# Kernel optimization log

Measured on AMD Instinct MI355X. Metric: run time of the kernel, lower is better.

## Reference

```python
import jax, jax.numpy as jnp
import numpy as np

E = 2048      # embed_dim
HQ = 32       # num_query_heads
HKV = 8       # num_kv_heads
DH = E // HQ  # head_dim = 64
G = HQ // HKV # group_size = 4
KV_DIM = E * HKV // HQ  # 512
B, S = 2, 2048


def setup_inputs() -> dict:
    key = jax.random.key(0)
    ks = jax.random.split(key, 11)
    sc_in = 1.0 / np.sqrt(E)
    sc_attn = 1.0 / np.sqrt(E)
    return {
        "query": jax.random.normal(ks[0], (B, S, E), jnp.float32),
        "key": jax.random.normal(ks[1], (B, S, E), jnp.float32),
        "value": jax.random.normal(ks[2], (B, S, E), jnp.float32),
        "Wq": jax.random.normal(ks[3], (E, E), jnp.float32) * sc_in,
        "bq": jnp.zeros((E,), jnp.float32),
        "Wk": jax.random.normal(ks[4], (E, KV_DIM), jnp.float32) * sc_in,
        "bk": jnp.zeros((KV_DIM,), jnp.float32),
        "Wv": jax.random.normal(ks[5], (E, KV_DIM), jnp.float32) * sc_in,
        "bv": jnp.zeros((KV_DIM,), jnp.float32),
        "Wo": jax.random.normal(ks[6], (E, E), jnp.float32) * sc_attn,
        "bo": jnp.zeros((E,), jnp.float32),
    }


def reference(query, key, value, Wq, bq, Wk, bk, Wv, bv, Wo, bo):
    b, s, _ = query.shape
    # projections
    Q = (query @ Wq + bq).reshape(b, s, HQ, DH).transpose(0, 2, 1, 3)   # [B,HQ,S,DH]
    K = (key @ Wk + bk).reshape(b, s, HKV, DH).transpose(0, 2, 1, 3)    # [B,HKV,S,DH]
    V = (value @ Wv + bv).reshape(b, s, HKV, DH).transpose(0, 2, 1, 3)  # [B,HKV,S,DH]
    # GQA: repeat_interleave along head dim (kv head h -> query heads h*G..h*G+G-1)
    K = jnp.repeat(K, G, axis=1)  # [B,HQ,S,DH]
    V = jnp.repeat(V, G, axis=1)  # [B,HQ,S,DH]
    scores = jnp.einsum('bhqd,bhkd->bhqk', Q, K) / np.sqrt(DH).astype(np.float32)
    attn_weights = jax.nn.softmax(scores, axis=-1)                      # [B,HQ,S,S]
    attn_out = jnp.einsum('bhqk,bhkd->bhqd', attn_weights, V)           # [B,HQ,S,DH]
    attn_out = attn_out.transpose(0, 2, 1, 3).reshape(b, s, E)
    out = attn_out @ Wo + bo
    return out, attn_weights
```

## Files before the change

### kernel.cpp

```cpp
#include <hip/hip_runtime.h>
#include <stdint.h>

typedef _Float16 f16;
typedef _Float16 f16x8 __attribute__((ext_vector_type(8)));
typedef _Float16 f16x4 __attribute__((ext_vector_type(4)));
typedef float    f32x4 __attribute__((ext_vector_type(4)));

#define SEQ   2048
#define EDIM  2048
#define NHQ   32
#define NHKV  8
#define DHEAD 64
#define KVD   512
#define NB    2
#define NTOK  (NB*SEQ)
#define SCALE 0.1803368801111204f

__device__ __forceinline__ f32x4 mfma16(f16x8 a, f16x8 b, f32x4 c) {
  return __builtin_amdgcn_mfma_f32_16x16x32_f16(a, b, c, 0, 0, 0);
}

__device__ __forceinline__ void gload_lds16(const void* g, void* l) {
  __builtin_amdgcn_global_load_lds(
      (const __attribute__((address_space(1))) void*)g,
      (__attribute__((address_space(3))) void*)l, 16, 0, 0);
}

__global__ __launch_bounds__(256) void k_cvt3(const float* __restrict__ s0,
                                              const float* __restrict__ s1,
                                              const float* __restrict__ s2,
                                              f16* __restrict__ d) {
  int i = blockIdx.x * 256 + threadIdx.x;
  int t = i >> 21, j = i & ((1 << 21) - 1);
  const float* s = (t == 0) ? s0 : ((t == 1) ? s1 : s2);
  float4 v = reinterpret_cast<const float4*>(s)[j];
  f16x4 h;
  h[0] = (f16)v.x; h[1] = (f16)v.y; h[2] = (f16)v.z; h[3] = (f16)v.w;
  reinterpret_cast<f16x4*>(d)[i] = h;
}

__global__ __launch_bounds__(256) void k_tconv(const float* __restrict__ s0,
                                               const float* __restrict__ s1,
                                               f16* __restrict__ d0,
                                               f16* __restrict__ d1,
                                               int R, int C) {
  const float* s = blockIdx.z ? s1 : s0;
  f16* d = blockIdx.z ? d1 : d0;
  __shared__ float t[32][33];
  int tr = blockIdx.x, tc = blockIdx.y;
  int lr = threadIdx.x >> 3;
  int lc = (threadIdx.x & 7) << 2;
  float4 v = *reinterpret_cast<const float4*>(&s[(size_t)(tr*32+lr)*C + tc*32 + lc]);
  t[lr][lc+0] = v.x; t[lr][lc+1] = v.y; t[lr][lc+2] = v.z; t[lr][lc+3] = v.w;
  __syncthreads();
  f16x4 h;
  h[0] = (f16)t[lc+0][lr];
  h[1] = (f16)t[lc+1][lr];
  h[2] = (f16)t[lc+2][lr];
  h[3] = (f16)t[lc+3][lr];
  *reinterpret_cast<f16x4*>(&d[(size_t)(tc*32+lr)*R + tr*32 + lc]) = h;
}

__global__ __launch_bounds__(256) void k_trv(const f16* __restrict__ src,
                                             f16* __restrict__ dst) {
  __shared__ f16 t[64][68];
  int bh = blockIdx.x;
  int st = blockIdx.y;
  int b = bh >> 3, h = bh & 7;
  #pragma unroll
  for (int i = 0; i < 4; ++i) {
    int sl = i*16 + (threadIdx.x >> 4);
    int d4 = (threadIdx.x & 15) * 4;
    *(f16x4*)&t[sl][d4] =
        *(const f16x4*)&src[(size_t)(b*SEQ + st*64 + sl)*KVD + h*DHEAD + d4];
  }
  __syncthreads();
  #pragma unroll
  for (int i = 0; i < 4; ++i) {
    int dl = i*16 + (threadIdx.x >> 4);
    int s4 = (threadIdx.x & 15) * 4;
    f16x4 v;
    v[0] = t[s4+0][dl]; v[1] = t[s4+1][dl]; v[2] = t[s4+2][dl]; v[3] = t[s4+3][dl];
    *(f16x4*)&dst[(size_t)(bh*DHEAD + dl)*SEQ + st*64 + s4] = v;
  }
}

template<int F16OUT>
__global__ __launch_bounds__(256) void k_gemm(
    const f16* __restrict__ A0, const f16* __restrict__ A1,
    const f16* __restrict__ Bt0, const f16* __restrict__ Bt1,
    const float* __restrict__ bias0, const float* __restrict__ bias1,
    void* __restrict__ C0, void* __restrict__ C1,
    int M, int N, int K)
{
  const f16* A    = blockIdx.z ? A1 : A0;
  const f16* Bt   = blockIdx.z ? Bt1 : Bt0;
  const float* bias = blockIdx.z ? bias1 : bias0;
  void* Cout      = blockIdx.z ? C1 : C0;

  __shared__ f16 sA[128*64];
  __shared__ f16 sB[128*64];
  const int tid  = threadIdx.x;
  const int lane = tid & 63, wv = tid >> 6;
  const int tn = blockIdx.x, tm = blockIdx.y;
  const int wm = wv >> 1, wn = wv & 1;
  const int l15 = lane & 15, lhi = lane >> 4;

  const f32x4 zz = {0.f, 0.f, 0.f, 0.f};
  f32x4 acc[4][4];
  #pragma unroll
  for (int m = 0; m < 4; ++m)
    #pragma unroll
    for (int n = 0; n < 4; ++n) acc[m][n] = zz;

  const f16* gsrc[8];
  f16* ldst[8];
  #pragma unroll
  for (int i = 0; i < 8; ++i) {
    int u = wv*8 + i;
    int r  = (u & 15)*8 + (lane >> 3);
    int cb = ((lane & 7) << 4) ^ ((r & 7) << 4);
    if (u < 16) {
      gsrc[i] = A  + (size_t)(tm*128 + r)*K + (cb >> 1);
      ldst[i] = sA + u*512;
    } else {
      gsrc[i] = Bt + (size_t)(tn*128 + r)*K + (cb >> 1);
      ldst[i] = sB + (u - 16)*512;
    }
  }

  int aoff[2][4], boff[2][4];
  #pragma unroll
  for (int ks = 0; ks < 2; ++ks)
    #pragma unroll
    for (int m = 0; m < 4; ++m) {
      int ra = wm*64 + m*16 + l15;
      aoff[ks][m] = ra*128 + ((ks*64 + (lhi << 4)) ^ ((ra & 7) << 4));
      int rb = wn*64 + m*16 + l15;
      boff[ks][m] = rb*128 + ((ks*64 + (lhi << 4)) ^ ((rb & 7) << 4));
    }

  const int nkb = K >> 6;
  for (int kb = 0; kb < nkb; ++kb) {
    #pragma unroll
    for (int i = 0; i < 8; ++i)
      gload_lds16(gsrc[i] + kb*64, ldst[i]);
    __syncthreads();
    #pragma unroll
    for (int ks = 0; ks < 2; ++ks) {
      f16x8 af[4], bf[4];
      #pragma unroll
      for (int m = 0; m < 4; ++m)
        af[m] = *(const f16x8*)((const char*)sA + aoff[ks][m]);
      #pragma unroll
      for (int n = 0; n < 4; ++n)
        bf[n] = *(const f16x8*)((const char*)sB + boff[ks][n]);
      #pragma unroll
      for (int m = 0; m < 4; ++m)
        #pragma unroll
        for (int n = 0; n < 4; ++n)
          acc[m][n] = mfma16(af[m], bf[n], acc[m][n]);
    }
    __syncthreads();
  }

  float bcol[4];
  #pragma unroll
  for (int n = 0; n < 4; ++n)
    bcol[n] = bias[tn*128 + wn*64 + n*16 + l15];
  #pragma unroll
  for (int m = 0; m < 4; ++m)
    #pragma unroll
    for (int n = 0; n < 4; ++n)
      #pragma unroll
      for (int r = 0; r < 4; ++r) {
        int row = tm*128 + wm*64 + m*16 + lhi*4 + r;
        int col = tn*128 + wn*64 + n*16 + l15;
        float v = acc[m][n][r] + bcol[n];
        if (F16OUT) ((f16*)Cout)[(size_t)row*N + col] = (f16)v;
        else        ((float*)Cout)[(size_t)row*N + col] = v;
      }
}

__global__ __launch_bounds__(256) void k_attn(
    const f16* __restrict__ Qp,
    const f16* __restrict__ Kp,
    const f16* __restrict__ Vt,
    float* __restrict__ wout,
    f16* __restrict__ AO)
{
  __shared__ f16 sK[2][64*64];
  __shared__ f16 sV[2][64*64];
  __shared__ f16 sW[4][16*64];
  const int tid = threadIdx.x, lane = tid & 63, wv = tid >> 6;
  const int bid = (blockIdx.x & 7) * 256 + (blockIdx.x >> 3);
  const int b = bid >> 10, h = (bid >> 5) & 31, qb = bid & 31;
  const int hk = h >> 2;
  const int l15 = lane & 15, lhi = lane >> 4;
  const int rloc = (lane >> 3) & 7, chk = lane & 7;
  const int csw = (chk ^ rloc) * 8;
  const int sw  = (l15 & 7) << 4;
  const int qrow0 = qb*64 + wv*16;
  const f32x4 zz = {0.f, 0.f, 0.f, 0.f};

  f16x8 qf[2];
  #pragma unroll
  for (int ks = 0; ks < 2; ++ks)
    qf[ks] = *(const f16x8*)&Qp[(size_t)(b*SEQ + qrow0 + l15)*EDIM
                                + h*DHEAD + ks*32 + lhi*8];

  const f16* Kb = Kp + (size_t)(b*SEQ)*KVD + hk*DHEAD;
  const f16* Vb = Vt + (size_t)((b*NHKV + hk)*DHEAD)*SEQ;

  float lsum = 0.f;
  {
    #pragma unroll
    for (int i = 0; i < 2; ++i) {
      int u = wv*2 + i;
      gload_lds16(Kb + (size_t)(u*8 + rloc)*KVD + csw, &sK[0][u*512]);
    }
    __syncthreads();
    int buf = 0;
    for (int kb = 0; kb < SEQ/64; ++kb) {
      if (kb < SEQ/64 - 1) {
        #pragma unroll
        for (int i = 0; i < 2; ++i) {
          int u = wv*2 + i;
          gload_lds16(Kb + (size_t)((kb+1)*64 + u*8 + rloc)*KVD + csw, &sK[buf^1][u*512]);
        }
      }
      #pragma unroll
      for (int kt = 0; kt < 4; ++kt) {
        const char* kbase = (const char*)&sK[buf][0] + (kt*16 + l15)*128;
        f16x8 kf0 = *(const f16x8*)(kbase + ((lhi*16) ^ sw));
        f16x8 kf1 = *(const f16x8*)(kbase + ((64 + lhi*16) ^ sw));
        f32x4 s = zz;
        s = mfma16(kf0, qf[0], s);
        s = mfma16(kf1, qf[1], s);
        #pragma unroll
        for (int r = 0; r < 4; ++r)
          lsum += __builtin_amdgcn_exp2f(s[r] * SCALE);
      }
      __syncthreads();
      buf ^= 1;
    }
  }
  float den = lsum;
  den += __shfl_xor(den, 16);
  den += __shfl_xor(den, 32);
  const float rinv = __builtin_amdgcn_rcpf(den);

  f32x4 o[4];
  #pragma unroll
  for (int dt = 0; dt < 4; ++dt) o[dt] = zz;

  f16* swv = &sW[wv][0];
  float* wrow = wout + (size_t)((b*NHQ + h)*SEQ + qrow0)*SEQ;

  {
    #pragma unroll
    for (int i = 0; i < 2; ++i) {
      int u = wv*2 + i;
      gload_lds16(Kb + (size_t)(u*8 + rloc)*KVD + csw, &sK[0][u*512]);
      gload_lds16(Vb + (size_t)(u*8 + rloc)*SEQ + csw, &sV[0][u*512]);
    }
    __syncthreads();
    int buf = 0;
    for (int kb = 0; kb < SEQ/64; ++kb) {
      if (kb < SEQ/64 - 1) {
        #pragma unroll
        for (int i = 0; i < 2; ++i) {
          int u = wv*2 + i;
          gload_lds16(Kb + (size_t)((kb+1)*64 + u*8 + rloc)*KVD + csw, &sK[buf^1][u*512]);
          gload_lds16(Vb + (size_t)(u*8 + rloc)*SEQ + (kb+1)*64 + csw, &sV[buf^1][u*512]);
        }
      }
      #pragma unroll
      for (int kt = 0; kt < 4; ++kt) {
        const char* kbase = (const char*)&sK[buf][0] + (kt*16 + l15)*128;
        f16x8 kf0 = *(const f16x8*)(kbase + ((lhi*16) ^ sw));
        f16x8 kf1 = *(const f16x8*)(kbase + ((64 + lhi*16) ^ sw));
        f32x4 s = zz;
        s = mfma16(kf0, qf[0], s);
        s = mfma16(kf1, qf[1], s);
        f32x4 wvec;
        f16x4 wh;
        #pragma unroll
        for (int r = 0; r < 4; ++r) {
          float w = __builtin_amdgcn_exp2f(s[r] * SCALE) * rinv;
          wvec[r] = w;
          wh[r] = (f16)w;
        }
        __builtin_nontemporal_store(wvec,
            (f32x4*)(wrow + (size_t)l15*SEQ + kb*64 + kt*16 + lhi*4));
        *(f16x4*)((char*)swv + l15*128 + ((kt*32 + lhi*8) ^ sw)) = wh;
      }
      #pragma unroll
      for (int ks = 0; ks < 2; ++ks) {
        f16x8 af = *(const f16x8*)((const char*)swv + l15*128 + ((ks*64 + lhi*16) ^ sw));
        #pragma unroll
        for (int dt = 0; dt < 4; ++dt) {
          const char* vbase = (const char*)&sV[buf][0] + (dt*16 + l15)*128;
          f16x8 vf = *(const f16x8*)(vbase + ((ks*64 + lhi*16) ^ sw));
          o[dt] = mfma16(af, vf, o[dt]);
        }
      }
      __syncthreads();
      buf ^= 1;
    }
  }

  #pragma unroll
  for (int dt = 0; dt < 4; ++dt)
    #pragma unroll
    for (int r = 0; r < 4; ++r)
      AO[(size_t)(b*SEQ + qrow0 + lhi*4 + r)*EDIM + h*DHEAD + dt*16 + l15]
          = (f16)o[dt][r];
}

extern "C" void kernel_launch(void* const* d_in, const int* in_sizes, int n_in,
                              void* d_out, int out_size, void* d_ws, size_t ws_size,
                              hipStream_t stream) {
  (void)in_sizes; (void)n_in; (void)out_size; (void)ws_size;
  const float* query = (const float*)d_in[0];
  const float* key   = (const float*)d_in[1];
  const float* value = (const float*)d_in[2];
  const float* Wq    = (const float*)d_in[3];
  const float* bq    = (const float*)d_in[4];
  const float* Wk    = (const float*)d_in[5];
  const float* bk    = (const float*)d_in[6];
  const float* Wv    = (const float*)d_in[7];
  const float* bv    = (const float*)d_in[8];
  const float* Wo    = (const float*)d_in[9];
  const float* bo    = (const float*)d_in[10];

  float* out   = (float*)d_out;
  float* wattn = out + (size_t)NTOK*EDIM;

  f16* p   = (f16*)d_ws;
  f16* q16 = p;  p += (size_t)NTOK*EDIM;
  f16* k16 = p;  p += (size_t)NTOK*EDIM;
  f16* v16 = p;  p += (size_t)NTOK*EDIM;
  f16* wqT = p;  p += (size_t)EDIM*EDIM;
  f16* wkT = p;  p += (size_t)KVD*EDIM;
  f16* wvT = p;  p += (size_t)KVD*EDIM;
  f16* woT = p;  p += (size_t)EDIM*EDIM;
  f16* Qp  = p;  p += (size_t)NTOK*EDIM;
  f16* Kp  = p;  p += (size_t)NTOK*KVD;
  f16* Vp  = p;  p += (size_t)NTOK*KVD;
  f16* Vt  = p;  p += (size_t)NTOK*KVD;
  f16* AO  = p;  p += (size_t)NTOK*EDIM;

  k_cvt3<<<3*(NTOK*EDIM/4)/256, 256, 0, stream>>>(query, key, value, q16);

  k_tconv<<<dim3(EDIM/32, EDIM/32, 2), 256, 0, stream>>>(Wq, Wo, wqT, woT, EDIM, EDIM);
  k_tconv<<<dim3(EDIM/32, KVD/32, 2),  256, 0, stream>>>(Wk, Wv, wkT, wvT, EDIM, KVD);

  k_gemm<1><<<dim3(EDIM/128, NTOK/128, 1), 256, 0, stream>>>(
      q16, q16, wqT, wqT, bq, bq, Qp, Qp, NTOK, EDIM, EDIM);
  k_gemm<1><<<dim3(KVD/128, NTOK/128, 2), 256, 0, stream>>>(
      k16, v16, wkT, wvT, bk, bv, Kp, Vp, NTOK, KVD, EDIM);

  k_trv<<<dim3(NB*NHKV, SEQ/64), 256, 0, stream>>>(Vp, Vt);

  k_attn<<<NB*NHQ*(SEQ/64), 256, 0, stream>>>(Qp, Kp, Vt, wattn, AO);

  k_gemm<0><<<dim3(EDIM/128, NTOK/128, 1), 256, 0, stream>>>(
      AO, AO, woT, woT, bo, bo, out, out, NTOK, EDIM, EDIM);
}
```

Baseline: 508.5 us.

## Fuse QKV projection GEMM and process two query tiles per attention wave

The three projection GEMMs become one launch that writes a packed QKV buffer, using contiguous weight layouts and per-column-tile input and bias selection. The attention kernel now handles 32 query rows per wave (128 per block), so each K and V tile loaded into LDS is reused for twice as many queries, halving K/V traffic and block count. It also swaps __syncthreads for a partial vmcnt wait plus barrier and adds sched barriers. The costs are higher register pressure (launch_bounds 256,4), fewer blocks, and reliance on the weight transposes being contiguous in workspace.

```diff
diff --git a/kernel.cpp b/kernel.cpp
--- a/kernel.cpp
+++ b/kernel.cpp
@@ -14,6 +14,7 @@
 #define KVD   512
 #define NB    2
 #define NTOK  (NB*SEQ)
+#define QKVN  3072
 #define SCALE 0.1803368801111204f
 
 __device__ __forceinline__ f32x4 mfma16(f16x8 a, f16x8 b, f32x4 c) {
@@ -61,7 +62,7 @@
   *reinterpret_cast<f16x4*>(&d[(size_t)(tc*32+lr)*R + tr*32 + lc]) = h;
 }
 
-__global__ __launch_bounds__(256) void k_trv(const f16* __restrict__ src,
+__global__ __launch_bounds__(256) void k_trv(const f16* __restrict__ qkv,
                                              f16* __restrict__ dst) {
   __shared__ f16 t[64][68];
   int bh = blockIdx.x;
@@ -72,7 +73,7 @@
     int sl = i*16 + (threadIdx.x >> 4);
     int d4 = (threadIdx.x & 15) * 4;
     *(f16x4*)&t[sl][d4] =
-        *(const f16x4*)&src[(size_t)(b*SEQ + st*64 + sl)*KVD + h*DHEAD + d4];
+        *(const f16x4*)&qkv[(size_t)(b*SEQ + st*64 + sl)*QKVN + 2560 + h*DHEAD + d4];
   }
   __syncthreads();
   #pragma unroll
@@ -85,19 +86,104 @@
   }
 }
 
-template<int F16OUT>
+__global__ __launch_bounds__(256) void k_gemm_qkv(
+    const f16* __restrict__ Abase,
+    const f16* __restrict__ Wt,
+    const float* __restrict__ bq, const float* __restrict__ bk,
+    const float* __restrict__ bv,
+    f16* __restrict__ Cout)
+{
+  const int tn = blockIdx.x, tm = blockIdx.y;
+  const int sel = (tn >= 16) + (tn >= 20);
+  const f16* A = Abase + (size_t)sel*NTOK*EDIM;
+  const float* bias = sel == 0 ? bq : (sel == 1 ? bk : bv);
+  const int coff = sel == 0 ? 0 : (sel == 1 ? 2048 : 2560);
+
+  __shared__ f16 sA[128*64];
+  __shared__ f16 sB[128*64];
+  const int tid  = threadIdx.x;
+  const int lane = tid & 63, wv = tid >> 6;
+  const int wm = wv >> 1, wn = wv & 1;
+  const int l15 = lane & 15, lhi = lane >> 4;
+
+  const f32x4 zz = {0.f, 0.f, 0.f, 0.f};
+  f32x4 acc[4][4];
+  #pragma unroll
+  for (int m = 0; m < 4; ++m)
+    #pragma unroll
+    for (int n = 0; n < 4; ++n) acc[m][n] = zz;
+
+  const f16* gsrc[8];
+  f16* ldst[8];
+  #pragma unroll
+  for (int i = 0; i < 8; ++i) {
+    int u = wv*8 + i;
+    int r  = (u & 15)*8 + (lane >> 3);
+    int cb = ((lane & 7) << 4) ^ ((r & 7) << 4);
+    if (u < 16) {
+      gsrc[i] = A  + (size_t)(tm*128 + r)*EDIM + (cb >> 1);
+      ldst[i] = sA + u*512;
+    } else {
+      gsrc[i] = Wt + (size_t)(tn*128 + r)*EDIM + (cb >> 1);
+      ldst[i] = sB + (u - 16)*512;
+    }
+  }
+
+  int aoff[2][4], boff[2][4];
+  #pragma unroll
+  for (int ks = 0; ks < 2; ++ks)
+    #pragma unroll
+    for (int m = 0; m < 4; ++m) {
+      int ra = wm*64 + m*16 + l15;
+      aoff[ks][m] = ra*128 + ((ks*64 + (lhi << 4)) ^ ((ra & 7) << 4));
+      int rb = wn*64 + m*16 + l15;
+      boff[ks][m] = rb*128 + ((ks*64 + (lhi << 4)) ^ ((rb & 7) << 4));
+    }
+
+  for (int kb = 0; kb < EDIM/64; ++kb) {
+    #pragma unroll
+    for (int i = 0; i < 8; ++i)
+      gload_lds16(gsrc[i] + kb*64, ldst[i]);
+    __syncthreads();
+    #pragma unroll
+    for (int ks = 0; ks < 2; ++ks) {
+      f16x8 af[4], bf[4];
+      #pragma unroll
+      for (int m = 0; m < 4; ++m)
+        af[m] = *(const f16x8*)((const char*)sA + aoff[ks][m]);
+      #pragma unroll
+      for (int n = 0; n < 4; ++n)
+        bf[n] = *(const f16x8*)((const char*)sB + boff[ks][n]);
+      #pragma unroll
+      for (int m = 0; m < 4; ++m)
+        #pragma unroll
+        for (int n = 0; n < 4; ++n)
+          acc[m][n] = mfma16(af[m], bf[n], acc[m][n]);
+    }
+    __syncthreads();
+  }
+
+  float bcol[4];
+  #pragma unroll
+  for (int n = 0; n < 4; ++n)
+    bcol[n] = bias[tn*128 + wn*64 + n*16 + l15 - coff];
+  #pragma unroll
+  for (int m = 0; m < 4; ++m)
+    #pragma unroll
+    for (int n = 0; n < 4; ++n)
+      #pragma unroll
+      for (int r = 0; r < 4; ++r) {
+        int row = tm*128 + wm*64 + m*16 + lhi*4 + r;
+        int col = tn*128 + wn*64 + n*16 + l15;
+        Cout[(size_t)row*QKVN + col] = (f16)(acc[m][n][r] + bcol[n]);
+      }
+}
+
 __global__ __launch_bounds__(256) void k_gemm(
-    const f16* __restrict__ A0, const f16* __restrict__ A1,
-    const f16* __restrict__ Bt0, const f16* __restrict__ Bt1,
-    const float* __restrict__ bias0, const float* __restrict__ bias1,
-    void* __restrict__ C0, void* __restrict__ C1,
+    const f16* __restrict__ A, const f16* __restrict__ Bt,
+    const float* __restrict__ bias, float* __restrict__ Cout,
     int M, int N, int K)
 {
-  const f16* A    = blockIdx.z ? A1 : A0;
-  const f16* Bt   = blockIdx.z ? Bt1 : Bt0;
-  const float* bias = blockIdx.z ? bias1 : bias0;
-  void* Cout      = blockIdx.z ? C1 : C0;
-
   __shared__ f16 sA[128*64];
   __shared__ f16 sB[128*64];
   const int tid  = threadIdx.x;
@@ -176,15 +262,12 @@
       for (int r = 0; r < 4; ++r) {
         int row = tm*128 + wm*64 + m*16 + lhi*4 + r;
         int col = tn*128 + wn*64 + n*16 + l15;
-        float v = acc[m][n][r] + bcol[n];
-        if (F16OUT) ((f16*)Cout)[(size_t)row*N + col] = (f16)v;
-        else        ((float*)Cout)[(size_t)row*N + col] = v;
-      }
-}
-
-__global__ __launch_bounds__(256) void k_attn(
-    const f16* __restrict__ Qp,
-    const f16* __restrict__ Kp,
+        Cout[(size_t)row*N + col] = acc[m][n][r] + bcol[n];
+      }
+}
+
+__global__ __launch_bounds__(256, 4) void k_attn(
+    const f16* __restrict__ QKV,
     const f16* __restrict__ Vt,
     float* __restrict__ wout,
     f16* __restrict__ AO)
@@ -193,31 +276,33 @@
   __shared__ f16 sV[2][64*64];
   __shared__ f16 sW[4][16*64];
   const int tid = threadIdx.x, lane = tid & 63, wv = tid >> 6;
-  const int bid = (blockIdx.x & 7) * 256 + (blockIdx.x >> 3);
-  const int b = bid >> 10, h = (bid >> 5) & 31, qb = bid & 31;
+  const int bid = (blockIdx.x & 7) * 128 + (blockIdx.x >> 3);
+  const int b = bid >> 9, h = (bid >> 4) & 31, qb = bid & 15;
   const int hk = h >> 2;
   const int l15 = lane & 15, lhi = lane >> 4;
   const int rloc = (lane >> 3) & 7, chk = lane & 7;
   const int csw = (chk ^ rloc) * 8;
   const int sw  = (l15 & 7) << 4;
-  const int qrow0 = qb*64 + wv*16;
+  const int qrow0 = qb*128 + wv*32;
   const f32x4 zz = {0.f, 0.f, 0.f, 0.f};
 
-  f16x8 qf[2];
-  #pragma unroll
-  for (int ks = 0; ks < 2; ++ks)
-    qf[ks] = *(const f16x8*)&Qp[(size_t)(b*SEQ + qrow0 + l15)*EDIM
-                                + h*DHEAD + ks*32 + lhi*8];
-
-  const f16* Kb = Kp + (size_t)(b*SEQ)*KVD + hk*DHEAD;
+  f16x8 qf[2][2];
+  #pragma unroll
+  for (int qt = 0; qt < 2; ++qt)
+    #pragma unroll
+    for (int ks = 0; ks < 2; ++ks)
+      qf[qt][ks] = *(const f16x8*)&QKV[(size_t)(b*SEQ + qrow0 + qt*16 + l15)*QKVN
+                                       + h*DHEAD + ks*32 + lhi*8];
+
+  const f16* Kb = QKV + 2048 + (size_t)(b*SEQ)*QKVN + hk*DHEAD;
   const f16* Vb = Vt + (size_t)((b*NHKV + hk)*DHEAD)*SEQ;
 
-  float lsum = 0.f;
+  float lsum0 = 0.f, lsum1 = 0.f;
   {
     #pragma unroll
     for (int i = 0; i < 2; ++i) {
       int u = wv*2 + i;
-      gload_lds16(Kb + (size_t)(u*8 + rloc)*KVD + csw, &sK[0][u*512]);
+      gload_lds16(Kb + (size_t)(u*8 + rloc)*QKVN + csw, &sK[0][u*512]);
     }
     __syncthreads();
     int buf = 0;
@@ -226,7 +311,7 @@
         #pragma unroll
         for (int i = 0; i < 2; ++i) {
           int u = wv*2 + i;
-          gload_lds16(Kb + (size_t)((kb+1)*64 + u*8 + rloc)*KVD + csw, &sK[buf^1][u*512]);
+          gload_lds16(Kb + (size_t)((kb+1)*64 + u*8 + rloc)*QKVN + csw, &sK[buf^1][u*512]);
         }
       }
       #pragma unroll
@@ -234,25 +319,31 @@
         const char* kbase = (const char*)&sK[buf][0] + (kt*16 + l15)*128;
         f16x8 kf0 = *(const f16x8*)(kbase + ((lhi*16) ^ sw));
         f16x8 kf1 = *(const f16x8*)(kbase + ((64 + lhi*16) ^ sw));
-        f32x4 s = zz;
-        s = mfma16(kf0, qf[0], s);
-        s = mfma16(kf1, qf[1], s);
-        #pragma unroll
-        for (int r = 0; r < 4; ++r)
-          lsum += __builtin_amdgcn_exp2f(s[r] * SCALE);
+        f32x4 s0 = zz, s1 = zz;
+        s0 = mfma16(kf0, qf[0][0], s0);
+        s0 = mfma16(kf1, qf[0][1], s0);
+        s1 = mfma16(kf0, qf[1][0], s1);
+        s1 = mfma16(kf1, qf[1][1], s1);
+        #pragma unroll
+        for (int r = 0; r < 4; ++r) {
+          lsum0 += __builtin_amdgcn_exp2f(s0[r] * SCALE);
+          lsum1 += __builtin_amdgcn_exp2f(s1[r] * SCALE);
+        }
       }
       __syncthreads();
       buf ^= 1;
     }
   }
-  float den = lsum;
-  den += __shfl_xor(den, 16);
-  den += __shfl_xor(den, 32);
-  const float rinv = __builtin_amdgcn_rcpf(den);
-
-  f32x4 o[4];
-  #pragma unroll
-  for (int dt = 0; dt < 4; ++dt) o[dt] = zz;
+  lsum0 += __shfl_xor(lsum0, 16); lsum0 += __shfl_xor(lsum0, 32);
+  lsum1 += __shfl_xor(lsum1, 16); lsum1 += __shfl_xor(lsum1, 32);
+  const float rinv0 = __builtin_amdgcn_rcpf(lsum0);
+  const float rinv1 = __builtin_amdgcn_rcpf(lsum1);
+
+  f32x4 o[2][4];
+  #pragma unroll
+  for (int qt = 0; qt < 2; ++qt)
+    #pragma unroll
+    for (int dt = 0; dt < 4; ++dt) o[qt][dt] = zz;
 
   f16* swv = &sW[wv][0];
   float* wrow = wout + (size_t)((b*NHQ + h)*SEQ + qrow0)*SEQ;
@@ -261,39 +352,48 @@
     #pragma unroll
     for (int i = 0; i < 2; ++i) {
       int u = wv*2 + i;
-      gload_lds16(Kb + (size_t)(u*8 + rloc)*KVD + csw, &sK[0][u*512]);
+      gload_lds16(Kb + (size_t)(u*8 + rloc)*QKVN + csw, &sK[0][u*512]);
       gload_lds16(Vb + (size_t)(u*8 + rloc)*SEQ + csw, &sV[0][u*512]);
     }
-    __syncthreads();
+    asm volatile("s_waitcnt vmcnt(0)" ::: "memory");
+    __builtin_amdgcn_s_barrier();
     int buf = 0;
     for (int kb = 0; kb < SEQ/64; ++kb) {
       if (kb < SEQ/64 - 1) {
         #pragma unroll
         for (int i = 0; i < 2; ++i) {
           int u = wv*2 + i;
-          gload_lds16(Kb + (size_t)((kb+1)*64 + u*8 + rloc)*KVD + csw, &sK[buf^1][u*512]);
+          gload_lds16(Kb + (size_t)((kb+1)*64 + u*8 + rloc)*QKVN + csw, &sK[buf^1][u*512]);
           gload_lds16(Vb + (size_t)(u*8 + rloc)*SEQ + (kb+1)*64 + csw, &sV[buf^1][u*512]);
         }
       }
+      __builtin_amdgcn_sched_barrier(0);
+      f16x4 wh1sav[4];
       #pragma unroll
       for (int kt = 0; kt < 4; ++kt) {
         const char* kbase = (const char*)&sK[buf][0] + (kt*16 + l15)*128;
         f16x8 kf0 = *(const f16x8*)(kbase + ((lhi*16) ^ sw));
         f16x8 kf1 = *(const f16x8*)(kbase + ((64 + lhi*16) ^ sw));
-        f32x4 s = zz;
-        s = mfma16(kf0, qf[0], s);
-        s = mfma16(kf1, qf[1], s);
-        f32x4 wvec;
-        f16x4 wh;
+        f32x4 s0 = zz, s1 = zz;
+        s0 = mfma16(kf0, qf[0][0], s0);
+        s0 = mfma16(kf1, qf[0][1], s0);
+        s1 = mfma16(kf0, qf[1][0], s1);
+        s1 = mfma16(kf1, qf[1][1], s1);
+        f32x4 w0, w1;
+        f16x4 wh0, wh1;
         #pragma unroll
         for (int r = 0; r < 4; ++r) {
-          float w = __builtin_amdgcn_exp2f(s[r] * SCALE) * rinv;
-          wvec[r] = w;
-          wh[r] = (f16)w;
-        }
-        __builtin_nontemporal_store(wvec,
+          float a = __builtin_amdgcn_exp2f(s0[r] * SCALE) * rinv0;
+          float c = __builtin_amdgcn_exp2f(s1[r] * SCALE) * rinv1;
+          w0[r] = a; wh0[r] = (f16)a;
+          w1[r] = c; wh1[r] = (f16)c;
+        }
+        __builtin_nontemporal_store(w0,
             (f32x4*)(wrow + (size_t)l15*SEQ + kb*64 + kt*16 + lhi*4));
-        *(f16x4*)((char*)swv + l15*128 + ((kt*32 + lhi*8) ^ sw)) = wh;
+        __builtin_nontemporal_store(w1,
+            (f32x4*)(wrow + (size_t)(16 + l15)*SEQ + kb*64 + kt*16 + lhi*4));
+        *(f16x4*)((char*)swv + l15*128 + ((kt*32 + lhi*8) ^ sw)) = wh0;
+        wh1sav[kt] = wh1;
       }
       #pragma unroll
       for (int ks = 0; ks < 2; ++ks) {
@@ -302,20 +402,38 @@
         for (int dt = 0; dt < 4; ++dt) {
           const char* vbase = (const char*)&sV[buf][0] + (dt*16 + l15)*128;
           f16x8 vf = *(const f16x8*)(vbase + ((ks*64 + lhi*16) ^ sw));
-          o[dt] = mfma16(af, vf, o[dt]);
-        }
-      }
-      __syncthreads();
+          o[0][dt] = mfma16(af, vf, o[0][dt]);
+        }
+      }
+      #pragma unroll
+      for (int kt = 0; kt < 4; ++kt)
+        *(f16x4*)((char*)swv + l15*128 + ((kt*32 + lhi*8) ^ sw)) = wh1sav[kt];
+      #pragma unroll
+      for (int ks = 0; ks < 2; ++ks) {
+        f16x8 af = *(const f16x8*)((const char*)swv + l15*128 + ((ks*64 + lhi*16) ^ sw));
+        #pragma unroll
+        for (int dt = 0; dt < 4; ++dt) {
+          const char* vbase = (const char*)&sV[buf][0] + (dt*16 + l15)*128;
+          f16x8 vf = *(const f16x8*)(vbase + ((ks*64 + lhi*16) ^ sw));
+          o[1][dt] = mfma16(af, vf, o[1][dt]);
+        }
+      }
+      __builtin_amdgcn_sched_barrier(0);
+      asm volatile("s_waitcnt vmcnt(8)" ::: "memory");
+      __builtin_amdgcn_s_barrier();
+      __builtin_amdgcn_sched_barrier(0);
       buf ^= 1;
     }
   }
 
   #pragma unroll
-  for (int dt = 0; dt < 4; ++dt)
-    #pragma unroll
-    for (int r = 0; r < 4; ++r)
-      AO[(size_t)(b*SEQ + qrow0 + lhi*4 + r)*EDIM + h*DHEAD + dt*16 + l15]
-          = (f16)o[dt][r];
+  for (int qt = 0; qt < 2; ++qt)
+    #pragma unroll
+    for (int dt = 0; dt < 4; ++dt)
+      #pragma unroll
+      for (int r = 0; r < 4; ++r)
+        AO[(size_t)(b*SEQ + qrow0 + qt*16 + lhi*4 + r)*EDIM + h*DHEAD + dt*16 + l15]
+            = (f16)o[qt][dt][r];
 }
 
 extern "C" void kernel_launch(void* const* d_in, const int* in_sizes, int n_in,
@@ -337,34 +455,30 @@
   float* out   = (float*)d_out;
   float* wattn = out + (size_t)NTOK*EDIM;
 
-  f16* p   = (f16*)d_ws;
-  f16* q16 = p;  p += (size_t)NTOK*EDIM;
-  f16* k16 = p;  p += (size_t)NTOK*EDIM;
-  f16* v16 = p;  p += (size_t)NTOK*EDIM;
-  f16* wqT = p;  p += (size_t)EDIM*EDIM;
-  f16* wkT = p;  p += (size_t)KVD*EDIM;
-  f16* wvT = p;  p += (size_t)KVD*EDIM;
-  f16* woT = p;  p += (size_t)EDIM*EDIM;
-  f16* Qp  = p;  p += (size_t)NTOK*EDIM;
-  f16* Kp  = p;  p += (size_t)NTOK*KVD;
-  f16* Vp  = p;  p += (size_t)NTOK*KVD;
-  f16* Vt  = p;  p += (size_t)NTOK*KVD;
-  f16* AO  = p;  p += (size_t)NTOK*EDIM;
+  f16* p    = (f16*)d_ws;
+  f16* q16  = p;  p += (size_t)NTOK*EDIM;
+  f16* k16  = p;  p += (size_t)NTOK*EDIM;
+  f16* v16  = p;  p += (size_t)NTOK*EDIM;
+  f16* wqT  = p;  p += (size_t)EDIM*EDIM;
+  f16* wkT  = p;  p += (size_t)KVD*EDIM;
+  f16* wvT  = p;  p += (size_t)KVD*EDIM;
+  f16* woT  = p;  p += (size_t)EDIM*EDIM;
+  f16* QKVp = p;  p += (size_t)NTOK*QKVN;
+  f16* Vt   = p;  p += (size_t)NTOK*KVD;
+  f16* AO   = p;  p += (size_t)NTOK*EDIM;
 
   k_cvt3<<<3*(NTOK*EDIM/4)/256, 256, 0, stream>>>(query, key, value, q16);
 
   k_tconv<<<dim3(EDIM/32, EDIM/32, 2), 256, 0, stream>>>(Wq, Wo, wqT, woT, EDIM, EDIM);
   k_tconv<<<dim3(EDIM/32, KVD/32, 2),  256, 0, stream>>>(Wk, Wv, wkT, wvT, EDIM, KVD);
 
-  k_gemm<1><<<dim3(EDIM/128, NTOK/128, 1), 256, 0, stream>>>(
-      q16, q16, wqT, wqT, bq, bq, Qp, Qp, NTOK, EDIM, EDIM);
-  k_gemm<1><<<dim3(KVD/128, NTOK/128, 2), 256, 0, stream>>>(
-      k16, v16, wkT, wvT, bk, bv, Kp, Vp, NTOK, KVD, EDIM);
-
-  k_trv<<<dim3(NB*NHKV, SEQ/64), 256, 0, stream>>>(Vp, Vt);
-
-  k_attn<<<NB*NHQ*(SEQ/64), 256, 0, stream>>>(Qp, Kp, Vt, wattn, AO);
-
-  k_gemm<0><<<dim3(EDIM/128, NTOK/128, 1), 256, 0, stream>>>(
-      AO, AO, woT, woT, bo, bo, out, out, NTOK, EDIM, EDIM);
-}
+  k_gemm_qkv<<<dim3(QKVN/128, NTOK/128), 256, 0, stream>>>(
+      q16, wqT, bq, bk, bv, QKVp);
+
+  k_trv<<<dim3(NB*NHKV, SEQ/64), 256, 0, stream>>>(QKVp, Vt);
+
+  k_attn<<<NB*NHQ*(SEQ/128), 256, 0, stream>>>(QKVp, Vt, wattn, AO);
+
+  k_gemm<<<dim3(EDIM/128, NTOK/128), 256, 0, stream>>>(
+      AO, woT, bo, out, NTOK, EDIM, EDIM);
+}
```

After: 526.6 us. 1.04x slower.
